# Performance work log

Hardware: AMD Instinct MI355X
Metric: run time of the kernel (lower is better)

## Reference

```python
import jax, jax.numpy as jnp
import numpy as np

EPS = 1e-5

def _bn(x, g, b):
    # BatchNorm1d in training mode: biased batch variance, eps=1e-5
    mu = jnp.mean(x, axis=0)
    var = jnp.var(x, axis=0)
    return g * (x - mu) * jax.lax.rsqrt(var + EPS) + b

def _prelu(x, a):
    return jnp.where(x >= 0, x, a * x)

def setup_inputs() -> dict:
    key = jax.random.key(0)
    ks = jax.random.split(key, 32)
    B, MF, E = 4096, 128, 64
    f32 = jnp.float32

    def lin_w(k, o, i):
        bound = 1.0 / np.sqrt(i)
        return jax.random.uniform(k, (o, i), f32, -bound, bound)

    def lin_b(k, o, i):
        bound = 1.0 / np.sqrt(i)
        return jax.random.uniform(k, (o,), f32, -bound, bound)

    def exp_w(k, e, o, i):
        bound = 1.0 / np.sqrt(i)
        return jax.random.uniform(k, (e, o, i), f32, -bound, bound)

    def exp_b(k, e, o, i):
        bound = 1.0 / np.sqrt(i)
        return jax.random.uniform(k, (e, o), f32, -bound, bound)

    quarter = jnp.full((1,), 0.25, f32)  # PReLU default init
    return {
        'm0': jax.random.normal(ks[0], (B, MF), f32),
        'x0': jax.random.normal(ks[1], (B, 64), f32),
        'mW1': lin_w(ks[2], 256, 128), 'mb1': lin_b(ks[3], 256, 128),
        'mg1': jnp.ones((256,), f32), 'mbe1': jnp.zeros((256,), f32), 'ma1': quarter,
        'mW2': lin_w(ks[4], 128, 256), 'mb2': lin_b(ks[5], 128, 256),
        'mg2': jnp.ones((128,), f32), 'mbe2': jnp.zeros((128,), f32), 'ma2': quarter,
        'mW3': lin_w(ks[6], 64, 128), 'mb3': lin_b(ks[7], 64, 128),
        'mg3': jnp.ones((64,), f32), 'mbe3': jnp.zeros((64,), f32), 'ma3': quarter,
        'Wenc0': exp_w(ks[8], E, 256, 64), 'benc0': exp_b(ks[9], E, 256, 64),
        'Wenc1': exp_w(ks[10], E, 256, 256), 'benc1': exp_b(ks[11], E, 256, 256),
        'Wdec0': exp_w(ks[12], E, 256, 256), 'bdec0': exp_b(ks[13], E, 256, 256),
        'Wdec1': exp_w(ks[14], E, 64, 256), 'bdec1': exp_b(ks[15], E, 64, 256),
        'bng': jnp.ones((256,), f32), 'bnb': jnp.zeros((256,), f32), 'a': quarter,
    }

def reference(m0, x0, mW1, mb1, mg1, mbe1, ma1, mW2, mb2, mg2, mbe2, ma2,
              mW3, mb3, mg3, mbe3, ma3, Wenc0, benc0, Wenc1, benc1,
              Wdec0, bdec0, Wdec1, bdec1, bng, bnb, a):
    # m_encoder (MNet): Linear+BN+PReLU x3 -> per-sample expert weights [B, 64]
    h = _prelu(_bn(m0 @ mW1.T + mb1, mg1, mbe1), ma1)
    h = _prelu(_bn(h @ mW2.T + mb2, mg2, mbe2), ma2)
    w = _prelu(_bn(h @ mW3.T + mb3, mg3, mbe3), ma3)  # [B, E]

    w_sum = jnp.sum(w)           # scalar sum over all B*E, as in torch code
    wn = w / w_sum               # [B, E]

    def experts(z, W, b):
        # all-experts dense combine: sum_e wn[b,e] * (z @ W_e^T + b_e)
        h = jnp.einsum('bi,eoi->beo', z, W) + b  # [B, E, O]
        return jnp.einsum('beo,be->bo', h, wn)

    # encoder: depth=2, BN+PReLU after each layer (shared bn(256) and PReLU)
    z = _prelu(_bn(experts(x0, Wenc0, benc0), bng, bnb), a)
    z = _prelu(_bn(experts(z, Wenc1, benc1), bng, bnb), a)
    # decoder: BN+PReLU on all but last layer
    y = _prelu(_bn(experts(z, Wdec0, bdec0), bng, bnb), a)
    y = experts(y, Wdec1, bdec1)  # [B, 64]
    return y
```

## Files before the change

kernel.cpp:

```cpp
#include <hip/hip_runtime.h>
#include <stdint.h>

#define BATCH 4096
#define NEXP 64

typedef __bf16 bf16x8 __attribute__((ext_vector_type(8)));
typedef float f32x4 __attribute__((ext_vector_type(4)));
typedef float f32x8 __attribute__((ext_vector_type(8)));
typedef unsigned int u32x4 __attribute__((ext_vector_type(4)));
typedef unsigned short u16x4 __attribute__((ext_vector_type(4)));
typedef unsigned short u16x8 __attribute__((ext_vector_type(8)));

__device__ __forceinline__ unsigned short f2bf(float f) {
  unsigned u = __builtin_bit_cast(unsigned, f);
  u += 0x7fffu + ((u >> 16) & 1u);
  return (unsigned short)(u >> 16);
}
__device__ __forceinline__ float bf2f(unsigned short h) {
  unsigned u = ((unsigned)h) << 16;
  return __builtin_bit_cast(float, u);
}

__device__ __forceinline__ void async_copy16(const void* g, void* l) {
  __builtin_amdgcn_global_load_lds(
      (const __attribute__((address_space(1))) void*)(uintptr_t)g,
      (__attribute__((address_space(3))) void*)(uintptr_t)l, 16, 0, 0);
}

enum { AM_PLAIN = 0, AM_BN = 1 };

template <int BM_, int BN_, int WR, int WC, int AMODE>
__global__ __launch_bounds__(256, 4) void gemm_k(
    const float* __restrict__ Af32, const float* __restrict__ scv,
    const float* __restrict__ shv, const float* __restrict__ alphaPtr,
    const unsigned short* __restrict__ PB, int K, int nsubsTot,
    float* __restrict__ Cp, const float* __restrict__ biasv, int N,
    int ktilesTot) {
  constexpr int MS = BM_ / 16;
  constexpr int NS = BN_ / 16;
  constexpr int WTM = BM_ / WR, WTN = BN_ / WC;
  constexpr int TM = WTM / 16, TN = WTN / 16;
  constexpr int PCH = MS / 2;

  __shared__ __align__(16) unsigned short As[2 * MS * 512];
  __shared__ __align__(16) unsigned short Bs[2 * NS * 512];

  const int tid = threadIdx.x;
  const int lane = tid & 63;
  const int wid = tid >> 6;
  const int wrow = wid / WC, wcol = wid % WC;

  const int m0 = blockIdx.x * BM_;
  const int ntile = blockIdx.y;
  const int n0 = ntile * BN_;

  float alpha = 0.f;
  if constexpr (AMODE == AM_BN) alpha = alphaPtr[0];

  f32x4 acc[TM][TN] = {};

  for (int kt = 0; kt < ktilesTot; ++kt) {
    const int k0 = kt * 64;

    for (int f = wid; f < 2 * NS; f += 4) {
      const int fkt = f / NS, fns = f % NS;
      const long fragIdx = (long)(k0 / 32 + fkt) * nsubsTot + (ntile * NS + fns);
      async_copy16(PB + fragIdx * 512 + lane * 8, &Bs[f * 512 + lane * 8]);
    }

#pragma unroll
    for (int p = 0; p < PCH; ++p) {
      const int id = p * 256 + tid;
      const int fA = id >> 6;
      const int q = id & 63;
      const int ksh = fA / MS, msub = fA % MS;
      const int kq = q >> 4, mrow = q & 15;
      const int m = msub * 16 + mrow;
      const int kg = k0 + ksh * 32 + kq * 8;
      const long mg = m0 + m;
      f32x8 vf;
      if constexpr (AMODE == AM_PLAIN) {
        const f32x4* src = (const f32x4*)(Af32 + mg * K + kg);
        f32x4 a0 = src[0], a1 = src[1];
#pragma unroll
        for (int j = 0; j < 4; ++j) { vf[j] = a0[j]; vf[4 + j] = a1[j]; }
      } else {
        const f32x4* src = (const f32x4*)(Af32 + mg * K + kg);
        f32x4 a0 = src[0], a1 = src[1];
        f32x4 s0 = *(const f32x4*)(scv + kg), s1 = *(const f32x4*)(scv + kg + 4);
        f32x4 h0 = *(const f32x4*)(shv + kg), h1 = *(const f32x4*)(shv + kg + 4);
#pragma unroll
        for (int j = 0; j < 4; ++j) {
          float v = fmaf(a0[j], s0[j], h0[j]);
          vf[j] = v >= 0.f ? v : alpha * v;
          float v2 = fmaf(a1[j], s1[j], h1[j]);
          vf[4 + j] = v2 >= 0.f ? v2 : alpha * v2;
        }
      }
      bf16x8 ob = __builtin_convertvector(vf, bf16x8);
      *(u16x8*)&As[id * 8] = __builtin_bit_cast(u16x8, ob);
    }
    __syncthreads();

#pragma unroll
    for (int ks = 0; ks < 2; ++ks) {
      bf16x8 af[TM], bfr[TN];
#pragma unroll
      for (int i = 0; i < TM; ++i) {
        const int msub = wrow * TM + i;
        af[i] = __builtin_bit_cast(
            bf16x8, *(const u32x4*)&As[(ks * MS + msub) * 512 + lane * 8]);
      }
#pragma unroll
      for (int j = 0; j < TN; ++j) {
        const int nsub = wcol * TN + j;
        bfr[j] = __builtin_bit_cast(
            bf16x8, *(const u32x4*)&Bs[(ks * NS + nsub) * 512 + lane * 8]);
      }
#pragma unroll
      for (int i = 0; i < TM; ++i)
#pragma unroll
        for (int j = 0; j < TN; ++j)
          acc[i][j] = __builtin_amdgcn_mfma_f32_16x16x32_bf16(af[i], bfr[j],
                                                              acc[i][j], 0, 0, 0);
    }
    __syncthreads();
  }

  const int q = lane >> 4, nn = lane & 15;
#pragma unroll
  for (int i = 0; i < TM; ++i) {
    const int rowb = m0 + wrow * WTM + i * 16 + q * 4;
#pragma unroll
    for (int j = 0; j < TN; ++j) {
      const int col = n0 + wcol * WTN + j * 16 + nn;
      const float bv = biasv ? biasv[col] : 0.f;
#pragma unroll
      for (int r = 0; r < 4; ++r)
        Cp[(long)(rowb + r) * N + col] = acc[i][j][r] + bv;
    }
  }
}

template <int BN_, int KE_, int EPB>
__global__ __launch_bounds__(256, 2) void egemm_k(
    const unsigned short* __restrict__ zpk, const float* __restrict__ wnT,
    const float* __restrict__ bias, const unsigned short* __restrict__ PB,
    float* __restrict__ Cbase, long partStride, int N, int nsubsTot) {
  constexpr int KT2 = KE_ / 32;
  constexpr int NS = BN_ / 16;
  constexpr int TN = NS / 4;
  constexpr int TM = 4;
  constexpr int MS = 4;

  const int tid = threadIdx.x, lane = tid & 63, wid = tid >> 6;
  const int mb = blockIdx.x, ntile = blockIdx.y, slice = blockIdx.z;
  const int e0 = slice * EPB;
  const int n0 = ntile * BN_;
  float* __restrict__ Cp = Cbase + (long)slice * partStride;
  const int nn = lane & 15, q = lane >> 4;

  u32x4 areg[TM][KT2];
  {
    const unsigned short* zb = zpk + (long)mb * (KT2 * MS * 512);
#pragma unroll
    for (int i = 0; i < TM; ++i)
#pragma unroll
      for (int kt = 0; kt < KT2; ++kt)
        areg[i][kt] = *(const u32x4*)(zb + (kt * MS + i) * 512 + lane * 8);
  }

  const unsigned short* Bw = PB + ((long)ntile * NS + wid * TN) * 512 + lane * 8;
  const long kstride = (long)nsubsTot * 512;

  f32x4 mainAcc[TM][TN] = {};
  u32x4 breg[2][TN];

#pragma unroll
  for (int j = 0; j < TN; ++j)
    breg[0][j] = *(const u32x4*)(Bw + (long)e0 * KT2 * kstride + j * 512);

  for (int ei = 0; ei < EPB; ++ei) {
    const int e = e0 + ei;
    float bv[TN];
#pragma unroll
    for (int j = 0; j < TN; ++j)
      bv[j] = bias[(long)e * N + n0 + wid * (TN * 16) + j * 16 + nn];
    f32x4 tmp[TM][TN];
#pragma unroll
    for (int i = 0; i < TM; ++i)
#pragma unroll
      for (int j = 0; j < TN; ++j) {
        f32x4 t = {bv[j], bv[j], bv[j], bv[j]};
        tmp[i][j] = t;
      }
#pragma unroll
    for (int kt = 0; kt < KT2; ++kt) {
      const int cur = kt & 1, nxt = cur ^ 1;
      if (kt + 1 < KT2 || ei + 1 < EPB) {
        const long tnext = (long)e * KT2 + kt + 1;
#pragma unroll
        for (int j = 0; j < TN; ++j)
          breg[nxt][j] = *(const u32x4*)(Bw + tnext * kstride + j * 512);
      }
#pragma unroll
      for (int i = 0; i < TM; ++i) {
        bf16x8 af = __builtin_bit_cast(bf16x8, areg[i][kt]);
#pragma unroll
        for (int j = 0; j < TN; ++j)
          tmp[i][j] = __builtin_amdgcn_mfma_f32_16x16x32_bf16(
              af, __builtin_bit_cast(bf16x8, breg[cur][j]), tmp[i][j], 0, 0, 0);
      }
    }
#pragma unroll
    for (int i = 0; i < TM; ++i) {
      const int rowb = mb * 64 + i * 16 + q * 4;
      f32x4 wn4 = *(const f32x4*)(wnT + (long)e * BATCH + rowb);
#pragma unroll
      for (int j = 0; j < TN; ++j) mainAcc[i][j] += wn4 * tmp[i][j];
    }
  }

#pragma unroll
  for (int i = 0; i < TM; ++i) {
    const int rowb = mb * 64 + i * 16 + q * 4;
#pragma unroll
    for (int j = 0; j < TN; ++j) {
      const int col = n0 + wid * (TN * 16) + j * 16 + nn;
#pragma unroll
      for (int r = 0; r < 4; ++r)
        Cp[(long)(rowb + r) * N + col] = mainAcc[i][j][r];
    }
  }
}

__global__ void hbuild_k(float* __restrict__ P, long partStride, int nparts,
                         int total4) {
  const int idx = blockIdx.x * 256 + threadIdx.x;
  if (idx >= total4) return;
  f32x4 s = *(const f32x4*)(P + (long)idx * 4);
  for (int p = 1; p < nparts; ++p)
    s += *(const f32x4*)(P + p * partStride + (long)idx * 4);
  *(f32x4*)(P + (long)idx * 4) = s;
}

__global__ void stats_k(const float* __restrict__ H, int C,
                        const float* __restrict__ g, const float* __restrict__ b,
                        float* __restrict__ scv, float* __restrict__ shv) {
  const int c0 = blockIdx.x * 4;
  f32x4 s = {0.f, 0.f, 0.f, 0.f}, s2 = {0.f, 0.f, 0.f, 0.f};
  for (int r = threadIdx.x; r < BATCH; r += 256) {
    f32x4 x = *(const f32x4*)(H + (long)r * C + c0);
    s += x;
    s2 += x * x;
  }
  __shared__ f32x4 sb[256], qb[256];
  sb[threadIdx.x] = s;
  qb[threadIdx.x] = s2;
  __syncthreads();
  for (int st = 128; st > 0; st >>= 1) {
    if (threadIdx.x < st) {
      sb[threadIdx.x] += sb[threadIdx.x + st];
      qb[threadIdx.x] += qb[threadIdx.x + st];
    }
    __syncthreads();
  }
  if (threadIdx.x < 4) {
    const int c = c0 + threadIdx.x;
    float mu = sb[0][threadIdx.x] * (1.f / BATCH);
    float var = qb[0][threadIdx.x] * (1.f / BATCH) - mu * mu;
    float isig = 1.f / sqrtf(var + 1e-5f);
    float sc_ = g[c] * isig;
    scv[c] = sc_;
    shv[c] = b[c] - mu * sc_;
  }
}

__global__ void zbuild_pk(const float* __restrict__ H,
                          const float* __restrict__ scv,
                          const float* __restrict__ shv,
                          const float* __restrict__ alphaPtr,
                          unsigned short* __restrict__ zpk) {
  const int c = blockIdx.x * 256 + threadIdx.x;
  const float alpha = alphaPtr[0];
  const int mb = c >> 11, r = c & 2047;
  const int kt = r >> 8, q2 = r & 255;
  const int msub = q2 >> 6, ln = q2 & 63;
  const int row = mb * 64 + msub * 16 + (ln & 15);
  const int col = kt * 32 + (ln >> 4) * 8;
  const float* src = H + (long)row * 256 + col;
  f32x4 a0 = *(const f32x4*)src, a1 = *(const f32x4*)(src + 4);
  f32x4 s0 = *(const f32x4*)(scv + col), s1 = *(const f32x4*)(scv + col + 4);
  f32x4 h0 = *(const f32x4*)(shv + col), h1 = *(const f32x4*)(shv + col + 4);
  u16x8 o;
#pragma unroll
  for (int j = 0; j < 4; ++j) {
    float v = fmaf(a0[j], s0[j], h0[j]);
    v = v >= 0.f ? v : alpha * v;
    o[j] = f2bf(v);
    float v2 = fmaf(a1[j], s1[j], h1[j]);
    v2 = v2 >= 0.f ? v2 : alpha * v2;
    o[4 + j] = f2bf(v2);
  }
  *(u16x8*)(zpk + (long)c * 8) = o;
}

__global__ void cast_pk(const float* __restrict__ x,
                        unsigned short* __restrict__ zpk) {
  const int c = blockIdx.x * 256 + threadIdx.x;
  const int mb = c >> 9, r = c & 511;
  const int kt = r >> 8, q2 = r & 255;
  const int msub = q2 >> 6, ln = q2 & 63;
  const int row = mb * 64 + msub * 16 + (ln & 15);
  const int col = kt * 32 + (ln >> 4) * 8;
  const float* src = x + (long)row * 64 + col;
  f32x4 a0 = *(const f32x4*)src, a1 = *(const f32x4*)(src + 4);
  u16x8 o;
#pragma unroll
  for (int j = 0; j < 4; ++j) {
    o[j] = f2bf(a0[j]);
    o[4 + j] = f2bf(a1[j]);
  }
  *(u16x8*)(zpk + (long)c * 8) = o;
}

__global__ void wbuild_k(const float* __restrict__ G, const float* __restrict__ scv,
                         const float* __restrict__ shv,
                         const float* __restrict__ alphaPtr,
                         float* __restrict__ w, float* __restrict__ wsum) {
  const int idx = blockIdx.x * 256 + threadIdx.x;
  const float alpha = alphaPtr[0];
  const int c0 = (idx * 4) & 63;
  f32x4 x = *(const f32x4*)(G + (long)idx * 4);
  f32x4 sv = *(const f32x4*)(scv + c0);
  f32x4 hv = *(const f32x4*)(shv + c0);
  f32x4 o;
  float part = 0.f;
#pragma unroll
  for (int j = 0; j < 4; ++j) {
    float v = fmaf(x[j], sv[j], hv[j]);
    v = v >= 0.f ? v : alpha * v;
    o[j] = v;
    part += v;
  }
  *(f32x4*)(w + (long)idx * 4) = o;
  __shared__ float sb[256];
  sb[threadIdx.x] = part;
  __syncthreads();
  for (int st = 128; st > 0; st >>= 1) {
    if (threadIdx.x < st) sb[threadIdx.x] += sb[threadIdx.x + st];
    __syncthreads();
  }
  if (threadIdx.x == 0) atomicAdd(wsum, sb[0]);
}

__global__ void inv_k(const float* __restrict__ wsum, float* __restrict__ invp) {
  if (threadIdx.x == 0 && blockIdx.x == 0) invp[0] = 1.0f / wsum[0];
}

__global__ void wntbuild_k(const float* __restrict__ w,
                           const float* __restrict__ invp,
                           float* __restrict__ wnT) {
  const int idx = blockIdx.x * 256 + threadIdx.x;
  const int e = idx >> 12, b = idx & 4095;
  wnT[idx] = w[(long)b * NEXP + e] * invp[0];
}

__global__ void prepack_k(const float* __restrict__ W, const float* __restrict__ bias,
                          unsigned short* __restrict__ PB, int O, int shI, int EI,
                          long totalChunks) {
  const long t = (long)blockIdx.x * 256 + threadIdx.x;
  if (t >= totalChunks) return;
  const int lane = (int)(t & 63);
  const long frag = t >> 6;
  const int nsubs = O / 16;
  const int nsub = (int)(frag % nsubs);
  const long ktile = frag / nsubs;
  const int n = nsub * 16 + (lane & 15);
  const int k = (int)(ktile * 32 + (lane >> 4) * 8);
  u16x8 o;
  if (k < EI) {
    const int e = k >> shI;
    const int i0 = k & ((1 << shI) - 1);
    const float* src = W + ((long)e * O + n) * (1 << shI) + i0;
    f32x4 a0 = *(const f32x4*)src;
    f32x4 a1 = *(const f32x4*)(src + 4);
#pragma unroll
    for (int j = 0; j < 4; ++j) {
      o[j] = f2bf(a0[j]);
      o[4 + j] = f2bf(a1[j]);
    }
  } else {
#pragma unroll
    for (int j = 0; j < 8; ++j) {
      const int ee = k + j - EI;
      o[j] = f2bf(bias[(long)ee * O + n]);
    }
  }
  *(u16x8*)(PB + t * 8) = o;
}

__global__ void reduceN_k(const float* __restrict__ P, long partStride, int nparts,
                          float* __restrict__ out, int total4) {
  const int idx = blockIdx.x * 256 + threadIdx.x;
  if (idx >= total4) return;
  f32x4 s = {0.f, 0.f, 0.f, 0.f};
  for (int p = 0; p < nparts; ++p) s += *(const f32x4*)(P + p * partStride + (long)idx * 4);
  *(f32x4*)(out + (long)idx * 4) = s;
}

extern "C" void kernel_launch(void* const* d_in, const int* in_sizes, int n_in,
                              void* d_out, int out_size, void* d_ws, size_t ws_size,
                              hipStream_t stream) {
  const float* m0 = (const float*)d_in[0];
  const float* x0 = (const float*)d_in[1];
  const float* mW1 = (const float*)d_in[2];
  const float* mb1 = (const float*)d_in[3];
  const float* mg1 = (const float*)d_in[4];
  const float* mbe1 = (const float*)d_in[5];
  const float* ma1 = (const float*)d_in[6];
  const float* mW2 = (const float*)d_in[7];
  const float* mb2 = (const float*)d_in[8];
  const float* mg2 = (const float*)d_in[9];
  const float* mbe2 = (const float*)d_in[10];
  const float* ma2 = (const float*)d_in[11];
  const float* mW3 = (const float*)d_in[12];
  const float* mb3 = (const float*)d_in[13];
  const float* mg3 = (const float*)d_in[14];
  const float* mbe3 = (const float*)d_in[15];
  const float* ma3 = (const float*)d_in[16];
  const float* Wenc0 = (const float*)d_in[17];
  const float* benc0 = (const float*)d_in[18];
  const float* Wenc1 = (const float*)d_in[19];
  const float* benc1 = (const float*)d_in[20];
  const float* Wdec0 = (const float*)d_in[21];
  const float* bdec0 = (const float*)d_in[22];
  const float* Wdec1 = (const float*)d_in[23];
  const float* bdec1 = (const float*)d_in[24];
  const float* bng = (const float*)d_in[25];
  const float* bnb = (const float*)d_in[26];
  const float* aexp = (const float*)d_in[27];

  const int SPL = 4, SPLD = 8;

  char* base = (char*)d_ws;
  size_t off = 0;
  auto alloc = [&](size_t bytes) {
    void* p = base + off;
    off = (off + bytes + 255) & ~(size_t)255;
    return p;
  };
  unsigned short* PB = (unsigned short*)alloc(16448L * 256 * 2);
  float* Pb = (float*)alloc((size_t)SPL * BATCH * 256 * 4);
  float* P0 = Pb;
  float* P1 = Pb + (long)BATCH * 256;
  unsigned short* zApk = (unsigned short*)alloc(BATCH * 256 * 2);
  unsigned short* zBpk = (unsigned short*)alloc(BATCH * 256 * 2);
  unsigned short* x0pk = (unsigned short*)alloc(BATCH * 64 * 2);
  float* wbuf = (float*)alloc(BATCH * 64 * 4);
  float* wnT = (float*)alloc((size_t)NEXP * BATCH * 4);
  float* scv = (float*)alloc(256 * 4);
  float* shv = (float*)alloc(256 * 4);
  float* wsum = (float*)alloc(256);
  float* invp = (float*)alloc(256);

  const dim3 blk(256);
  const long PS = BATCH * 256;

  prepack_k<<<16, blk, 0, stream>>>(mW1, nullptr, PB, 256, 7, 128, 4096);
  gemm_k<64, 128, 2, 2, AM_PLAIN><<<dim3(64, 2, 1), blk, 0, stream>>>(
      m0, nullptr, nullptr, nullptr, PB, 128, 16, P0, mb1, 256, 2);
  stats_k<<<64, blk, 0, stream>>>(P0, 256, mg1, mbe1, scv, shv);

  prepack_k<<<16, blk, 0, stream>>>(mW2, nullptr, PB, 128, 8, 256, 4096);
  gemm_k<64, 128, 2, 2, AM_BN><<<dim3(64, 1, 1), blk, 0, stream>>>(
      P0, scv, shv, ma1, PB, 256, 8, P1, mb2, 128, 4);
  stats_k<<<32, blk, 0, stream>>>(P1, 128, mg2, mbe2, scv, shv);

  prepack_k<<<4, blk, 0, stream>>>(mW3, nullptr, PB, 64, 7, 128, 1024);
  gemm_k<64, 64, 2, 2, AM_BN><<<dim3(64, 1, 1), blk, 0, stream>>>(
      P1, scv, shv, ma2, PB, 128, 4, P0, mb3, 64, 2);
  stats_k<<<16, blk, 0, stream>>>(P0, 64, mg3, mbe3, scv, shv);

  hipMemsetAsync(wsum, 0, 4, stream);
  wbuild_k<<<256, blk, 0, stream>>>(P0, scv, shv, ma3, wbuf, wsum);
  inv_k<<<1, 64, 0, stream>>>(wsum, invp);
  wntbuild_k<<<1024, blk, 0, stream>>>(wbuf, invp, wnT);
  cast_pk<<<128, blk, 0, stream>>>(x0, x0pk);

  prepack_k<<<512, blk, 0, stream>>>(Wenc0, nullptr, PB, 256, 6, 4096, 131072);
  egemm_k<128, 64, 16><<<dim3(64, 2, SPL), blk, 0, stream>>>(
      x0pk, wnT, benc0, PB, Pb, PS, 256, 16);
  hbuild_k<<<1024, blk, 0, stream>>>(Pb, PS, SPL, 262144);
  stats_k<<<64, blk, 0, stream>>>(Pb, 256, bng, bnb, scv, shv);
  zbuild_pk<<<512, blk, 0, stream>>>(Pb, scv, shv, aexp, zApk);

  prepack_k<<<2048, blk, 0, stream>>>(Wenc1, nullptr, PB, 256, 8, 16384, 524288);
  egemm_k<128, 256, 16><<<dim3(64, 2, SPL), blk, 0, stream>>>(
      zApk, wnT, benc1, PB, Pb, PS, 256, 16);
  hbuild_k<<<1024, blk, 0, stream>>>(Pb, PS, SPL, 262144);
  stats_k<<<64, blk, 0, stream>>>(Pb, 256, bng, bnb, scv, shv);
  zbuild_pk<<<512, blk, 0, stream>>>(Pb, scv, shv, aexp, zBpk);

  prepack_k<<<2048, blk, 0, stream>>>(Wdec0, nullptr, PB, 256, 8, 16384, 524288);
  egemm_k<128, 256, 16><<<dim3(64, 2, SPL), blk, 0, stream>>>(
      zBpk, wnT, bdec0, PB, Pb, PS, 256, 16);
  hbuild_k<<<1024, blk, 0, stream>>>(Pb, PS, SPL, 262144);
  stats_k<<<64, blk, 0, stream>>>(Pb, 256, bng, bnb, scv, shv);
  zbuild_pk<<<512, blk, 0, stream>>>(Pb, scv, shv, aexp, zApk);

  prepack_k<<<512, blk, 0, stream>>>(Wdec1, nullptr, PB, 64, 8, 16384, 131072);
  egemm_k<64, 256, 8><<<dim3(64, 1, SPLD), blk, 0, stream>>>(
      zApk, wnT, bdec1, PB, Pb, (long)BATCH * 64, 64, 4);
  reduceN_k<<<256, blk, 0, stream>>>(Pb, (long)BATCH * 64, SPLD, (float*)d_out, 65536);

  (void)in_sizes; (void)n_in; (void)out_size; (void)ws_size;
}
```

Baseline: 409.2 us.

## Deepen expert-GEMM B prefetch to a 4-slot ring and double the expert splits

The expert GEMM kernel now streams B fragments through a 4-deep register ring instead of a 2-slot double buffer, so global loads are issued several k-steps ahead of the MFMAs that consume them. The launch becomes a 1D grid in which blocks that share the same row tile are adjacent, which should improve cache reuse of A and the weighted norms. Experts are split into twice as many slices (fewer experts per block), giving more parallel blocks. The cost is more partial-sum buffers for hbuild/reduce to read and write, and extra register pressure from the deeper ring.

```diff
diff --git a/kernel.cpp b/kernel.cpp
--- a/kernel.cpp
+++ b/kernel.cpp
@@ -142,7 +142,7 @@
   }
 }
 
-template <int BN_, int KE_, int EPB>
+template <int BN_, int KE_, int EPB, int NTILE>
 __global__ __launch_bounds__(256, 2) void egemm_k(
     const unsigned short* __restrict__ zpk, const float* __restrict__ wnT,
     const float* __restrict__ bias, const unsigned short* __restrict__ PB,
@@ -151,73 +151,82 @@
   constexpr int NS = BN_ / 16;
   constexpr int TN = NS / 4;
   constexpr int TM = 4;
-  constexpr int MS = 4;
+  constexpr int NC = NTILE * (NEXP / EPB);
+  constexpr int T = EPB * KT2;
+  constexpr int U = ((KT2 & 3) == 0) ? 1 : (4 / KT2);
 
   const int tid = threadIdx.x, lane = tid & 63, wid = tid >> 6;
-  const int mb = blockIdx.x, ntile = blockIdx.y, slice = blockIdx.z;
+  const int bx = blockIdx.x;
+  const int combo = bx % NC;
+  const int mb = bx / NC;
+  const int ntile = combo % NTILE;
+  const int slice = combo / NTILE;
   const int e0 = slice * EPB;
   const int n0 = ntile * BN_;
   float* __restrict__ Cp = Cbase + (long)slice * partStride;
   const int nn = lane & 15, q = lane >> 4;
 
+  const unsigned short* Aw = zpk + (long)mb * (KT2 * 4 * 512);
   u32x4 areg[TM][KT2];
-  {
-    const unsigned short* zb = zpk + (long)mb * (KT2 * MS * 512);
-#pragma unroll
-    for (int i = 0; i < TM; ++i)
-#pragma unroll
-      for (int kt = 0; kt < KT2; ++kt)
-        areg[i][kt] = *(const u32x4*)(zb + (kt * MS + i) * 512 + lane * 8);
-  }
-
-  const unsigned short* Bw = PB + ((long)ntile * NS + wid * TN) * 512 + lane * 8;
-  const long kstride = (long)nsubsTot * 512;
+#pragma unroll
+  for (int i = 0; i < TM; ++i)
+#pragma unroll
+    for (int kt = 0; kt < KT2; ++kt)
+      areg[i][kt] = *(const u32x4*)(Aw + (kt * 4 + i) * 512 + lane * 8);
+
+  const long kstr = (long)nsubsTot * 512;
+  const unsigned short* Bt = PB + (long)e0 * KT2 * kstr +
+                             ((long)ntile * NS + wid * TN) * 512 + lane * 8;
+
+  u32x4 ring[4][TN];
+#pragma unroll
+  for (int t = 0; t < 4; ++t)
+#pragma unroll
+    for (int j = 0; j < TN; ++j)
+      ring[t][j] = *(const u32x4*)(Bt + (long)t * kstr + j * 512);
 
   f32x4 mainAcc[TM][TN] = {};
-  u32x4 breg[2][TN];
-
-#pragma unroll
-  for (int j = 0; j < TN; ++j)
-    breg[0][j] = *(const u32x4*)(Bw + (long)e0 * KT2 * kstride + j * 512);
-
-  for (int ei = 0; ei < EPB; ++ei) {
-    const int e = e0 + ei;
-    float bv[TN];
-#pragma unroll
-    for (int j = 0; j < TN; ++j)
-      bv[j] = bias[(long)e * N + n0 + wid * (TN * 16) + j * 16 + nn];
-    f32x4 tmp[TM][TN];
-#pragma unroll
-    for (int i = 0; i < TM; ++i)
+
+  for (int eb = 0; eb < EPB; eb += U) {
+#pragma unroll
+    for (int u = 0; u < U; ++u) {
+      const int ei = eb + u;
+      const int e = e0 + ei;
+      f32x4 tmp[TM][TN];
 #pragma unroll
       for (int j = 0; j < TN; ++j) {
-        f32x4 t = {bv[j], bv[j], bv[j], bv[j]};
-        tmp[i][j] = t;
+        const float bv = bias[(long)e * N + n0 + wid * (TN * 16) + j * 16 + nn];
+        f32x4 t4 = {bv, bv, bv, bv};
+#pragma unroll
+        for (int i = 0; i < TM; ++i) tmp[i][j] = t4;
       }
 #pragma unroll
-    for (int kt = 0; kt < KT2; ++kt) {
-      const int cur = kt & 1, nxt = cur ^ 1;
-      if (kt + 1 < KT2 || ei + 1 < EPB) {
-        const long tnext = (long)e * KT2 + kt + 1;
-#pragma unroll
-        for (int j = 0; j < TN; ++j)
-          breg[nxt][j] = *(const u32x4*)(Bw + tnext * kstride + j * 512);
+      for (int kt = 0; kt < KT2; ++kt) {
+        const int slot = (u * KT2 + kt) & 3;
+#pragma unroll
+        for (int i = 0; i < TM; ++i) {
+          bf16x8 af = __builtin_bit_cast(bf16x8, areg[i][kt]);
+#pragma unroll
+          for (int j = 0; j < TN; ++j)
+            tmp[i][j] = __builtin_amdgcn_mfma_f32_16x16x32_bf16(
+                af, __builtin_bit_cast(bf16x8, ring[slot][j]), tmp[i][j], 0, 0,
+                0);
+        }
+        {
+          const int t = ei * KT2 + kt;
+          const int tl = (t + 4 < T) ? (t + 4) : (T - 1);
+#pragma unroll
+          for (int j = 0; j < TN; ++j)
+            ring[slot][j] = *(const u32x4*)(Bt + (long)tl * kstr + j * 512);
+        }
       }
 #pragma unroll
       for (int i = 0; i < TM; ++i) {
-        bf16x8 af = __builtin_bit_cast(bf16x8, areg[i][kt]);
-#pragma unroll
-        for (int j = 0; j < TN; ++j)
-          tmp[i][j] = __builtin_amdgcn_mfma_f32_16x16x32_bf16(
-              af, __builtin_bit_cast(bf16x8, breg[cur][j]), tmp[i][j], 0, 0, 0);
+        const int rowb = mb * 64 + i * 16 + q * 4;
+        f32x4 wn4 = *(const f32x4*)(wnT + (long)e * BATCH + rowb);
+#pragma unroll
+        for (int j = 0; j < TN; ++j) mainAcc[i][j] += wn4 * tmp[i][j];
       }
-    }
-#pragma unroll
-    for (int i = 0; i < TM; ++i) {
-      const int rowb = mb * 64 + i * 16 + q * 4;
-      f32x4 wn4 = *(const f32x4*)(wnT + (long)e * BATCH + rowb);
-#pragma unroll
-      for (int j = 0; j < TN; ++j) mainAcc[i][j] += wn4 * tmp[i][j];
     }
   }
 
@@ -441,7 +450,7 @@
   const float* bnb = (const float*)d_in[26];
   const float* aexp = (const float*)d_in[27];
 
-  const int SPL = 4, SPLD = 8;
+  const int SPL = 8, SPLD = 16;
 
   char* base = (char*)d_ws;
   size_t off = 0;
@@ -489,30 +498,31 @@
   cast_pk<<<128, blk, 0, stream>>>(x0, x0pk);
 
   prepack_k<<<512, blk, 0, stream>>>(Wenc0, nullptr, PB, 256, 6, 4096, 131072);
-  egemm_k<128, 64, 16><<<dim3(64, 2, SPL), blk, 0, stream>>>(
+  egemm_k<128, 64, 8, 2><<<dim3(1024), blk, 0, stream>>>(
       x0pk, wnT, benc0, PB, Pb, PS, 256, 16);
   hbuild_k<<<1024, blk, 0, stream>>>(Pb, PS, SPL, 262144);
   stats_k<<<64, blk, 0, stream>>>(Pb, 256, bng, bnb, scv, shv);
   zbuild_pk<<<512, blk, 0, stream>>>(Pb, scv, shv, aexp, zApk);
 
   prepack_k<<<2048, blk, 0, stream>>>(Wenc1, nullptr, PB, 256, 8, 16384, 524288);
-  egemm_k<128, 256, 16><<<dim3(64, 2, SPL), blk, 0, stream>>>(
+  egemm_k<128, 256, 8, 2><<<dim3(1024), blk, 0, stream>>>(
       zApk, wnT, benc1, PB, Pb, PS, 256, 16);
   hbuild_k<<<1024, blk, 0, stream>>>(Pb, PS, SPL, 262144);
   stats_k<<<64, blk, 0, stream>>>(Pb, 256, bng, bnb, scv, shv);
   zbuild_pk<<<512, blk, 0, stream>>>(Pb, scv, shv, aexp, zBpk);
 
   prepack_k<<<2048, blk, 0, stream>>>(Wdec0, nullptr, PB, 256, 8, 16384, 524288);
-  egemm_k<128, 256, 16><<<dim3(64, 2, SPL), blk, 0, stream>>>(
+  egemm_k<128, 256, 8, 2><<<dim3(1024), blk, 0, stream>>>(
       zBpk, wnT, bdec0, PB, Pb, PS, 256, 16);
   hbuild_k<<<1024, blk, 0, stream>>>(Pb, PS, SPL, 262144);
   stats_k<<<64, blk, 0, stream>>>(Pb, 256, bng, bnb, scv, shv);
   zbuild_pk<<<512, blk, 0, stream>>>(Pb, scv, shv, aexp, zApk);
 
   prepack_k<<<512, blk, 0, stream>>>(Wdec1, nullptr, PB, 64, 8, 16384, 131072);
-  egemm_k<64, 256, 8><<<dim3(64, 1, SPLD), blk, 0, stream>>>(
+  egemm_k<64, 256, 4, 1><<<dim3(1024), blk, 0, stream>>>(
       zApk, wnT, bdec1, PB, Pb, (long)BATCH * 64, 64, 4);
-  reduceN_k<<<256, blk, 0, stream>>>(Pb, (long)BATCH * 64, SPLD, (float*)d_out, 65536);
+  reduceN_k<<<256, blk, 0, stream>>>(Pb, (long)BATCH * 64, SPLD, (float*)d_out,
+                                     65536);
 
   (void)in_sizes; (void)n_in; (void)out_size; (void)ws_size;
 }
```

Result: no change. 410.5 us (+0.3%).
